# Optimization experiments

Hardware: AMD Instinct MI355X
Metric: run time of the kernel (lower is better)

## Reference

```python
import jax, jax.numpy as jnp
import numpy as np

HIDDEN = 512
HEADS = 8
HEAD_DIM = HIDDEN // HEADS
NUM_NODES = 512
NUM_EDGES = 16384
NEG_INF = -1e9


def setup_inputs() -> dict:
    key = jax.random.key(0)
    ks = jax.random.split(key, 8)
    x = jax.random.normal(ks[0], (4, 12, NUM_NODES, HIDDEN), dtype=jnp.float32)
    edge_index = jax.random.randint(ks[1], (2, NUM_EDGES), 0, NUM_NODES, dtype=jnp.int64)
    s = 1.0 / np.sqrt(HIDDEN)
    Wq = jax.random.uniform(ks[2], (HIDDEN, HIDDEN), jnp.float32, -s, s)
    Wk = jax.random.uniform(ks[3], (HIDDEN, HIDDEN), jnp.float32, -s, s)
    Wv = jax.random.uniform(ks[4], (HIDDEN, HIDDEN), jnp.float32, -s, s)
    bq = jax.random.uniform(ks[5], (HIDDEN,), jnp.float32, -s, s)
    bk = jax.random.uniform(ks[6], (HIDDEN,), jnp.float32, -s, s)
    bv = jax.random.uniform(ks[7], (HIDDEN,), jnp.float32, -s, s)
    return {"x": x, "edge_index": edge_index, "Wq": Wq, "bq": bq,
            "Wk": Wk, "bk": bk, "Wv": Wv, "bv": bv}


def reference(x, edge_index, Wq, bq, Wk, bk, Wv, bv):
    B, S, N, F = x.shape  # [batch, seq_len, num_nodes, features]
    xf = x.reshape(B * S, N, F)
    # torch nn.Linear: y = x @ W.T + b
    Q = xf @ Wq.T + bq
    K = xf @ Wk.T + bk
    V = xf @ Wv.T + bv
    # [B*S, heads, N, head_dim]
    Q = Q.reshape(B * S, N, HEADS, HEAD_DIM).transpose(0, 2, 1, 3)
    K = K.reshape(B * S, N, HEADS, HEAD_DIM).transpose(0, 2, 1, 3)
    V = V.reshape(B * S, N, HEADS, HEAD_DIM).transpose(0, 2, 1, 3)
    scores = jnp.einsum('bhnd,bhmd->bhnm', Q, K) / np.sqrt(HEAD_DIM)
    # static graph mask: 1 where edge exists
    mask = jnp.zeros((N, N), dtype=jnp.float32).at[edge_index[0], edge_index[1]].set(1.0)
    scores = jnp.where(mask[None, None] == 0, NEG_INF, scores)
    attn = jax.nn.softmax(scores, axis=-1)  # dropout is identity in eval
    out = jnp.einsum('bhnm,bhmd->bhnd', attn, V)
    out = out.transpose(0, 2, 1, 3).reshape(B, S, N, F)
    return out
```

## Files before the change

kernel.cpp:

```cpp
#include <hip/hip_runtime.h>
#include <hip/hip_bf16.h>

typedef __attribute__((ext_vector_type(8))) short short8;
typedef __attribute__((ext_vector_type(4))) float f32x4;
typedef __attribute__((ext_vector_type(4))) unsigned int u32x4;
typedef unsigned long long u64;
typedef unsigned short u16;
typedef unsigned int u32;

#define NODES 512
#define HIDDEN 512
#define NEDGES 16384

#define KOFF ((size_t)384 * 32 * 2 * 512)
#define VOFF ((size_t)2 * 384 * 32 * 2 * 512)

static __device__ __forceinline__ u16 f2bf(float f) {
  unsigned u = __float_as_uint(f);
  u += 0x7FFFu + ((u >> 16) & 1u);
  return (u16)(u >> 16);
}

static __device__ __forceinline__ void gld_lds16(const void* g, void* l) {
  __builtin_amdgcn_global_load_lds(
      (const __attribute__((address_space(1))) unsigned int*)g,
      (__attribute__((address_space(3))) unsigned int*)l, 16, 0, 0);
}

__global__ void cast_f32_bf16(const float* __restrict__ in, u16* __restrict__ out, int n4) {
  int stride = gridDim.x * blockDim.x;
  for (int i = blockIdx.x * blockDim.x + threadIdx.x; i < n4; i += stride) {
    float4 v = reinterpret_cast<const float4*>(in)[i];
    ushort4 o;
    o.x = f2bf(v.x); o.y = f2bf(v.y); o.z = f2bf(v.z); o.w = f2bf(v.w);
    reinterpret_cast<ushort4*>(out)[i] = o;
  }
}

__global__ void cast_w3(const float* __restrict__ a, const float* __restrict__ b,
                        const float* __restrict__ c, u16* __restrict__ out) {
  int i = blockIdx.x * blockDim.x + threadIdx.x;
  const float* src = (i < 65536) ? a : (i < 131072) ? b : c;
  float4 v = reinterpret_cast<const float4*>(src)[i & 65535];
  ushort4 o;
  o.x = f2bf(v.x); o.y = f2bf(v.y); o.z = f2bf(v.z); o.w = f2bf(v.w);
  reinterpret_cast<ushort4*>(out)[i] = o;
}

__global__ void mask_scatter(const int* __restrict__ e, u64* __restrict__ bits) {
  int i = blockIdx.x * blockDim.x + threadIdx.x;
  if (i < NEDGES) {
    int src = e[i];
    int dst = e[NEDGES + i];
    atomicOr(&bits[src * 8 + (dst >> 6)], 1ull << (dst & 63));
  }
}

__global__ void mask_frag(const u64* __restrict__ bits, u32* __restrict__ mf) {
  int idx = blockIdx.x * 256 + threadIdx.x;
  int w = idx & 3;
  int lane = (idx >> 2) & 63;
  int hh = (idx >> 8) & 1;
  int kt = (idx >> 9) & 7;
  int qsg = idx >> 12;
  int q = qsg * 16 + (lane & 15);
  int bit = hh * 32 + (lane >> 4) * 8 + 2 * w;
  u64 row = bits[q * 8 + kt];
  u32 b0 = (u32)(row >> bit) & 1u;
  u32 b1 = (u32)(row >> (bit + 1)) & 1u;
  mf[idx] = (b0 ? 0xFFFFu : 0u) | (b1 ? 0xFFFF0000u : 0u);
}

__global__ __launch_bounds__(256, 2)
void qkv_gemm(const u16* __restrict__ xb, const u16* __restrict__ wb,
              const float* __restrict__ bq, const float* __restrict__ bk,
              const float* __restrict__ bv, u16* __restrict__ qkv) {
  __shared__ u16 As[128 * 64];
  __shared__ u16 Bs[128 * 64];

  const int blk = blockIdx.x;
  const int xcd = blk & 7;
  const int i = blk >> 3;
  const int m0 = ((i % 24) + xcd * 24) * 128;
  const int nz = i / 24;
  const int n0 = (nz & 3) * 128;
  const int z = nz >> 2;

  const u16* Wz = wb + (size_t)z * (512 * 512);
  const float* bias = (z == 0) ? bq : (z == 1) ? bk : bv;

  const int tid = threadIdx.x;
  const int lane = tid & 63;
  const int w = tid >> 6;
  const int wr = w >> 1, wc = w & 1;
  const int l = lane & 15, j = lane >> 4;
  const int sl = l & 7;
  const int kb = ((lane & 7) ^ (lane >> 3)) * 16;

  f32x4 acc[4][4] = {};

  for (int kt = 0; kt < 8; ++kt) {
    const int k0 = kt * 64;
#pragma unroll
    for (int t = 0; t < 4; ++t) {
      int c = w * 4 + t;
      int row = c * 8 + (lane >> 3);
      gld_lds16((const char*)xb + ((size_t)(m0 + row) * 512 + k0) * 2 + kb,
                (char*)As + c * 1024);
      gld_lds16((const char*)Wz + ((size_t)(n0 + row) * 512 + k0) * 2 + kb,
                (char*)Bs + c * 1024);
    }
    __syncthreads();
#pragma unroll
    for (int kk = 0; kk < 2; ++kk) {
      short8 a[4], b[4];
#pragma unroll
      for (int mi = 0; mi < 4; ++mi)
        a[mi] = *(const short8*)(As + (wr * 64 + mi * 16 + l) * 64 +
                                 (((kk * 4 + j) ^ sl) * 8));
#pragma unroll
      for (int ni = 0; ni < 4; ++ni)
        b[ni] = *(const short8*)(Bs + (wc * 64 + ni * 16 + l) * 64 +
                                 (((kk * 4 + j) ^ sl) * 8));
      if (z == 2) {
#pragma unroll
        for (int mi = 0; mi < 4; ++mi)
#pragma unroll
          for (int ni = 0; ni < 4; ++ni)
            acc[mi][ni] = __builtin_amdgcn_mfma_f32_16x16x32_bf16(a[mi], b[ni], acc[mi][ni], 0, 0, 0);
      } else {
#pragma unroll
        for (int mi = 0; mi < 4; ++mi)
#pragma unroll
          for (int ni = 0; ni < 4; ++ni)
            acc[mi][ni] = __builtin_amdgcn_mfma_f32_16x16x32_bf16(b[ni], a[mi], acc[mi][ni], 0, 0, 0);
      }
    }
    __syncthreads();
  }

  const int bs = m0 >> 9;
  const int hh = (n0 >> 6) + wc;
  const int bh = bs * 8 + hh;

  if (z == 2) {
    const int ktb = ((m0 & 511) >> 6) + wr;
#pragma unroll
    for (int ni = 0; ni < 4; ++ni) {
      int jcol = n0 + wc * 64 + ni * 16 + l;
      float bv_ = bias[jcol];
      int ds = ni;
#pragma unroll
      for (int mi = 0; mi < 4; ++mi) {
        int kk2 = mi >> 1, oct = ((mi & 1) << 1) | (j >> 1);
        ushort4 pk;
#pragma unroll
        for (int r = 0; r < 4; ++r) pk[r] = f2bf(acc[mi][ni][r] + bv_);
        size_t idx = VOFF + (((((size_t)bh * 8 + ktb) * 2 + kk2) * 4 + ds) * 512)
                   + (oct * 16 + l) * 8 + (j & 1) * 4;
        *reinterpret_cast<ushort4*>(qkv + idx) = pk;
      }
    }
  } else {
#pragma unroll
    for (int ni = 0; ni < 4; ++ni) {
      int n_base = n0 + wc * 64 + ni * 16 + j * 4;
      float4 b4 = *reinterpret_cast<const float4*>(bias + n_base);
      int kk = ni >> 1, oct = ((ni & 1) << 1) | (j >> 1);
#pragma unroll
      for (int mi = 0; mi < 4; ++mi) {
        ushort4 pk;
#pragma unroll
        for (int r = 0; r < 4; ++r) pk[r] = f2bf(acc[mi][ni][r] + (&b4.x)[r]);
        size_t idx;
        if (z == 0) {
          int qsg = ((m0 & 511) >> 4) + wr * 4 + mi;
          idx = ((((size_t)bh * 32 + qsg) * 2 + kk) * 512) + (oct * 16 + l) * 8 + (j & 1) * 4;
        } else {
          int ktb = ((m0 & 511) >> 6) + wr;
          idx = KOFF + (((((size_t)bh * 8 + ktb) * 4 + mi) * 2 + kk) * 512)
              + (oct * 16 + l) * 8 + (j & 1) * 4;
        }
        *reinterpret_cast<ushort4*>(qkv + idx) = pk;
      }
    }
  }
}

__global__ __launch_bounds__(256, 2)
void attn_kernel(const u16* __restrict__ qkv, const u32* __restrict__ mf,
                 float* __restrict__ out) {
  const int blk = blockIdx.x;
  const int xcd = blk & 7;
  const int i = blk >> 3;
  const int bh = xcd * 48 + (i >> 2);
  const int qq = i & 3;
  const int bs = bh >> 3, h = bh & 7;
  const int tid = threadIdx.x;
  const int lane = tid & 63;
  const int w = tid >> 6;
  const int l = lane & 15, j = lane >> 4;
  const int qb = qq * 8 + w * 2;

  short8 qf[2][2];
#pragma unroll
  for (int qs = 0; qs < 2; ++qs)
#pragma unroll
    for (int kk = 0; kk < 2; ++kk)
      qf[qs][kk] = *(const short8*)(qkv + (((size_t)bh * 32 + qb + qs) * 2 + kk) * 512 + lane * 8);

  const u16* Kp = qkv + KOFF + (size_t)bh * 32768 + lane * 8;
  const u16* Vp = qkv + VOFF + (size_t)bh * 32768 + lane * 8;
  const u32* M0 = mf + (qb + 0) * 4096 + lane * 4;
  const u32* M1 = mf + (qb + 1) * 4096 + lane * 4;

  f32x4 o[2][4] = {};
  f32x4 osum[2] = {};
  short8 ones;
#pragma unroll
  for (int t = 0; t < 8; ++t) ones[t] = (short)0x3F80;

#pragma unroll 1
  for (int p = 0; p < 16; ++p) {
    short8 kf2[2][2];
#pragma unroll
    for (int lks = 0; lks < 2; ++lks)
#pragma unroll
      for (int kk = 0; kk < 2; ++kk)
        kf2[lks][kk] = *(const short8*)(Kp + (lks * 2 + kk) * 512);
    short8 vf[4];
#pragma unroll
    for (int ds = 0; ds < 4; ++ds)
      vf[ds] = *(const short8*)(Vp + ds * 512);
    u32x4 am0 = *reinterpret_cast<const u32x4*>(M0);
    u32x4 am1 = *reinterpret_cast<const u32x4*>(M1);

#pragma unroll
    for (int qs = 0; qs < 2; ++qs) {
      f32x4 st[2] = {};
#pragma unroll
      for (int lks = 0; lks < 2; ++lks)
#pragma unroll
        for (int kk = 0; kk < 2; ++kk)
          st[lks] = __builtin_amdgcn_mfma_f32_16x16x32_bf16(
              kf2[lks][kk], qf[qs][kk], st[lks], 0, 0, 0);

      float pr[8];
#pragma unroll
      for (int lks = 0; lks < 2; ++lks)
#pragma unroll
        for (int r = 0; r < 4; ++r)
          pr[lks * 4 + r] = __builtin_exp2f(st[lks][r] * 0.18033688f);
      u32 X0, X1, Y0, Y1;
      asm("v_cvt_pk_bf16_f32 %0, %1, %2" : "=v"(X0) : "v"(pr[0]), "v"(pr[1]));
      asm("v_cvt_pk_bf16_f32 %0, %1, %2" : "=v"(X1) : "v"(pr[2]), "v"(pr[3]));
      asm("v_cvt_pk_bf16_f32 %0, %1, %2" : "=v"(Y0) : "v"(pr[4]), "v"(pr[5]));
      asm("v_cvt_pk_bf16_f32 %0, %1, %2" : "=v"(Y1) : "v"(pr[6]), "v"(pr[7]));
      asm("v_permlane32_swap_b32 %0, %1" : "+v"(X0), "+v"(Y0));
      asm("v_permlane32_swap_b32 %0, %1" : "+v"(X1), "+v"(Y1));
      asm("v_permlane16_swap_b32 %0, %1" : "+v"(X0), "+v"(Y0));
      asm("v_permlane16_swap_b32 %0, %1" : "+v"(X1), "+v"(Y1));
      const u32x4 am = qs ? am1 : am0;
      u32x4 paw;
      paw[0] = X0 & am[0];
      paw[1] = X1 & am[1];
      paw[2] = Y0 & am[2];
      paw[3] = Y1 & am[3];
      short8 pa = __builtin_bit_cast(short8, paw);
      osum[qs] = __builtin_amdgcn_mfma_f32_16x16x32_bf16(pa, ones, osum[qs], 0, 0, 0);
#pragma unroll
      for (int ds = 0; ds < 4; ++ds)
        o[qs][ds] = __builtin_amdgcn_mfma_f32_16x16x32_bf16(pa, vf[ds], o[qs][ds], 0, 0, 0);
    }

    Kp += 2048; Vp += 2048; M0 += 256; M1 += 256;
  }

#pragma unroll
  for (int qs = 0; qs < 2; ++qs) {
    f32x4 inv4;
#pragma unroll
    for (int r = 0; r < 4; ++r) inv4[r] = 1.0f / osum[qs][r];
#pragma unroll
    for (int ds = 0; ds < 4; ++ds) {
      int d = ds * 16 + l;
#pragma unroll
      for (int r = 0; r < 4; ++r) {
        int node = (qb + qs) * 16 + j * 4 + r;
        out[(size_t)bs * 262144 + (size_t)node * 512 + h * 64 + d] = o[qs][ds][r] * inv4[r];
      }
    }
  }
}

extern "C" void kernel_launch(void* const* d_in, const int* in_sizes, int n_in,
                              void* d_out, int out_size, void* d_ws, size_t ws_size,
                              hipStream_t stream) {
  const float* x  = (const float*)d_in[0];
  const int*   e  = (const int*)d_in[1];
  const float* Wq = (const float*)d_in[2];
  const float* bq = (const float*)d_in[3];
  const float* Wk = (const float*)d_in[4];
  const float* bk = (const float*)d_in[5];
  const float* Wv = (const float*)d_in[6];
  const float* bv = (const float*)d_in[7];
  float* out = (float*)d_out;

  char* ws = (char*)d_ws;
  u16* xb   = (u16*)(ws);
  u16* wb   = (u16*)(ws + 25165824);
  u16* qkv  = (u16*)(ws + 26738688);
  u64* mb   = (u64*)(ws + 102236160);
  u32* mfr  = (u32*)(ws + 102268928);

  hipMemsetAsync(mb, 0, 512 * 8 * sizeof(u64), stream);
  mask_scatter<<<(NEDGES + 255) / 256, 256, 0, stream>>>(e, mb);
  mask_frag<<<512, 256, 0, stream>>>(mb, mfr);

  cast_f32_bf16<<<2048, 256, 0, stream>>>(x, xb, (24576 * 512) / 4);
  cast_w3<<<768, 256, 0, stream>>>(Wq, Wk, Wv, wb);

  qkv_gemm<<<2304, 256, 0, stream>>>(xb, wb, bq, bk, bv, qkv);
  attn_kernel<<<1536, 256, 0, stream>>>(qkv, mfr, out);
}
```

Baseline: 129.6 us.

## Double-buffer QKV GEMM LDS tiles and merge cast kernels into one

The QKV GEMM now keeps two LDS buffers for A and B and issues the global-to-LDS loads for the next k-tile before computing the current one. This overlaps memory latency with MFMA work and drops one barrier per iteration. LDS use doubles to 64KB per block, which may limit the 2-blocks-per-CU occupancy target. Separately, the x and weight cast kernels are merged into one grid-stride launch to save a kernel launch.

```diff
diff --git a/kernel.cpp b/kernel.cpp
--- a/kernel.cpp
+++ b/kernel.cpp
@@ -27,24 +27,28 @@
       (__attribute__((address_space(3))) unsigned int*)l, 16, 0, 0);
 }
 
-__global__ void cast_f32_bf16(const float* __restrict__ in, u16* __restrict__ out, int n4) {
+__global__ void cast_all(const float* __restrict__ x, const float* __restrict__ wq,
+                         const float* __restrict__ wk, const float* __restrict__ wv,
+                         u16* __restrict__ xb, u16* __restrict__ wb) {
+  const int n4 = 3145728 + 196608;
   int stride = gridDim.x * blockDim.x;
   for (int i = blockIdx.x * blockDim.x + threadIdx.x; i < n4; i += stride) {
-    float4 v = reinterpret_cast<const float4*>(in)[i];
+    float4 v;
+    u16* dst;
+    int di;
+    if (i < 3145728) {
+      v = reinterpret_cast<const float4*>(x)[i];
+      dst = xb; di = i;
+    } else {
+      int t = i - 3145728;
+      const float* src = (t < 65536) ? wq : (t < 131072) ? wk : wv;
+      v = reinterpret_cast<const float4*>(src)[t & 65535];
+      dst = wb; di = t;
+    }
     ushort4 o;
     o.x = f2bf(v.x); o.y = f2bf(v.y); o.z = f2bf(v.z); o.w = f2bf(v.w);
-    reinterpret_cast<ushort4*>(out)[i] = o;
-  }
-}
-
-__global__ void cast_w3(const float* __restrict__ a, const float* __restrict__ b,
-                        const float* __restrict__ c, u16* __restrict__ out) {
-  int i = blockIdx.x * blockDim.x + threadIdx.x;
-  const float* src = (i < 65536) ? a : (i < 131072) ? b : c;
-  float4 v = reinterpret_cast<const float4*>(src)[i & 65535];
-  ushort4 o;
-  o.x = f2bf(v.x); o.y = f2bf(v.y); o.z = f2bf(v.z); o.w = f2bf(v.w);
-  reinterpret_cast<ushort4*>(out)[i] = o;
+    reinterpret_cast<ushort4*>(dst)[di] = o;
+  }
 }
 
 __global__ void mask_scatter(const int* __restrict__ e, u64* __restrict__ bits) {
@@ -75,8 +79,8 @@
 void qkv_gemm(const u16* __restrict__ xb, const u16* __restrict__ wb,
               const float* __restrict__ bq, const float* __restrict__ bk,
               const float* __restrict__ bv, u16* __restrict__ qkv) {
-  __shared__ u16 As[128 * 64];
-  __shared__ u16 Bs[128 * 64];
+  __shared__ u16 As[2][128 * 64];
+  __shared__ u16 Bs[2][128 * 64];
 
   const int blk = blockIdx.x;
   const int xcd = blk & 7;
@@ -97,30 +101,37 @@
   const int sl = l & 7;
   const int kb = ((lane & 7) ^ (lane >> 3)) * 16;
 
+#define STAGE(bb, kt_) do {                                                     \
+    const int k0_ = (kt_) * 64;                                                 \
+    _Pragma("unroll")                                                           \
+    for (int t_ = 0; t_ < 4; ++t_) {                                            \
+      int c_ = w * 4 + t_;                                                      \
+      int row_ = c_ * 8 + (lane >> 3);                                          \
+      gld_lds16((const char*)xb + ((size_t)(m0 + row_) * 512 + k0_) * 2 + kb,   \
+                (char*)&As[bb][0] + c_ * 1024);                                 \
+      gld_lds16((const char*)Wz + ((size_t)(n0 + row_) * 512 + k0_) * 2 + kb,   \
+                (char*)&Bs[bb][0] + c_ * 1024);                                 \
+    }                                                                           \
+  } while (0)
+
   f32x4 acc[4][4] = {};
 
+  STAGE(0, 0);
+  __syncthreads();
+  int cur = 0;
+
   for (int kt = 0; kt < 8; ++kt) {
-    const int k0 = kt * 64;
-#pragma unroll
-    for (int t = 0; t < 4; ++t) {
-      int c = w * 4 + t;
-      int row = c * 8 + (lane >> 3);
-      gld_lds16((const char*)xb + ((size_t)(m0 + row) * 512 + k0) * 2 + kb,
-                (char*)As + c * 1024);
-      gld_lds16((const char*)Wz + ((size_t)(n0 + row) * 512 + k0) * 2 + kb,
-                (char*)Bs + c * 1024);
-    }
-    __syncthreads();
+    if (kt < 7) STAGE(cur ^ 1, kt + 1);
 #pragma unroll
     for (int kk = 0; kk < 2; ++kk) {
       short8 a[4], b[4];
 #pragma unroll
       for (int mi = 0; mi < 4; ++mi)
-        a[mi] = *(const short8*)(As + (wr * 64 + mi * 16 + l) * 64 +
+        a[mi] = *(const short8*)(&As[cur][0] + (wr * 64 + mi * 16 + l) * 64 +
                                  (((kk * 4 + j) ^ sl) * 8));
 #pragma unroll
       for (int ni = 0; ni < 4; ++ni)
-        b[ni] = *(const short8*)(Bs + (wc * 64 + ni * 16 + l) * 64 +
+        b[ni] = *(const short8*)(&Bs[cur][0] + (wc * 64 + ni * 16 + l) * 64 +
                                  (((kk * 4 + j) ^ sl) * 8));
       if (z == 2) {
 #pragma unroll
@@ -137,7 +148,9 @@
       }
     }
     __syncthreads();
-  }
+    cur ^= 1;
+  }
+#undef STAGE
 
   const int bs = m0 >> 9;
   const int hh = (n0 >> 6) + wc;
@@ -317,8 +330,7 @@
   mask_scatter<<<(NEDGES + 255) / 256, 256, 0, stream>>>(e, mb);
   mask_frag<<<512, 256, 0, stream>>>(mb, mfr);
 
-  cast_f32_bf16<<<2048, 256, 0, stream>>>(x, xb, (24576 * 512) / 4);
-  cast_w3<<<768, 256, 0, stream>>>(Wq, Wk, Wv, wb);
+  cast_all<<<2048, 256, 0, stream>>>(x, Wq, Wk, Wv, xb, wb);
 
   qkv_gemm<<<2304, 256, 0, stream>>>(xb, wb, bq, bk, bv, qkv);
   attn_kernel<<<1536, 256, 0, stream>>>(qkv, mfr, out);
```

New measurement: 127.1 us. No clear change (-1.9%).
